# Kernel optimization log

Hardware: AMD Instinct MI355X
Metric: run time of the kernel (lower is better)

## Reference

```python
import jax, jax.numpy as jnp
import numpy as np

# Static problem constants (see shape_source)
T_, H_, W_ = 8, 37, 37          # frames, feature-map height/width (518/14)
NH, MP = 8, 8                   # num_heads, max_points


def _point_mask_np():
    # n_points(t, r) = max(1, int(MP * (1 - |t-r|/(T-1)))) as in the TxT loop.
    d = np.abs(np.arange(T_)[:, None] - np.arange(T_)[None, :])
    n_p = np.maximum(1, (MP * (1.0 - d / (T_ - 1))).astype(np.int64))
    return np.arange(MP)[None, None, :] < n_p[:, :, None]   # [T, T, P] bool


def setup_inputs() -> dict:
    key = jax.random.key(0)
    ks = jax.random.split(key, 4)
    B, T, N, C = 2, T_, H_ * W_, 384
    f_bt = jax.random.normal(ks[0], (B, T, N, C), jnp.float32)
    Wq = 0.05 * jax.random.normal(ks[1], (C, C), jnp.float32)
    Woff = 0.1 * jax.random.normal(ks[2], (C, NH * MP * 2), jnp.float32)  # offsets span a few pixels
    Wout = 0.05 * jax.random.normal(ks[3], (C, C), jnp.float32)
    return {
        'f_bt': f_bt,
        'Wq': Wq, 'bq': jnp.zeros((C,), jnp.float32),
        'Woff': Woff, 'boff': jnp.zeros((NH * MP * 2,), jnp.float32),
        'Wout': Wout, 'bout': jnp.zeros((C,), jnp.float32),
    }


def _forward(f_bt, Wq, bq, Woff, boff, Wout, bout):
    B, T, N, C = f_bt.shape
    h, P = NH, MP
    hd = C // h
    scale = hd ** -0.5
    H, W = H_, W_

    # Per-frame projections (query and offsets depend only on t, computed once).
    q = (f_bt @ Wq + bq).reshape(B, T, N, h, hd)                 # [B,T,N,h,hd]
    off = (f_bt @ Woff + boff).reshape(B, T, N, h, P, 2)         # [B,T,N,h,P,2]

    ys, xs = jnp.meshgrid(jnp.arange(H), jnp.arange(W), indexing='ij')
    coords = jnp.stack([ys, xs], -1).reshape(N, 2).astype(f_bt.dtype)
    # Sampling locations in pixel space (align_corners=True normalize+denormalize is identity).
    loc = coords[None, None, :, None, None, :] + off             # [B,T,N,h,P,2]

    # Reference frames as per-head channel images, flattened spatially.
    ref = f_bt.transpose(0, 1, 3, 2).reshape(B, T, h, hd, N)     # [B,T,h,hd,H*W]
    mask = jnp.asarray(_point_mask_np())                         # [T,T,P]

    def attend(q_t, loc_t, mask_t):
        # q_t: [B,N,h,hd], loc_t: [B,N,h,P,2], mask_t: [T,P]
        y = loc_t[..., 0]
        x = loc_t[..., 1]
        y0f = jnp.floor(y)
        x0f = jnp.floor(x)
        wy = y - y0f
        wx = x - x0f

        def gather(yf, xf, w):
            yi = yf.astype(jnp.int32)
            xi = xf.astype(jnp.int32)
            valid = ((yi >= 0) & (yi < H) & (xi >= 0) & (xi < W)).astype(q_t.dtype)
            idx = jnp.clip(yi, 0, H - 1) * W + jnp.clip(xi, 0, W - 1)     # [B,N,h,P]
            idx = idx.transpose(0, 2, 1, 3).reshape(B, 1, h, 1, N * P)
            idx = jnp.broadcast_to(idx, (B, T, h, 1, N * P))
            vals = jnp.take_along_axis(ref, idx, axis=4)                   # [B,T,h,hd,N*P]
            vals = vals.reshape(B, T, h, hd, N, P)
            wv = (w * valid).transpose(0, 2, 1, 3)[:, None, :, None, :, :]  # [B,1,h,1,N,P]
            return vals * wv

        # Bilinear sample (zeros padding) of every reference frame at the
        # offset-predicted points of frame t.
        s = (gather(y0f, x0f, (1 - wy) * (1 - wx))
             + gather(y0f, x0f + 1, (1 - wy) * wx)
             + gather(y0f + 1, x0f, wy * (1 - wx))
             + gather(y0f + 1, x0f + 1, wy * wx))                # [B,T,h,hd,N,P]

        logits = jnp.einsum('bnhd,brhdnp->brnhp', q_t, s) * scale
        logits = logits + jnp.where(mask_t[None, :, None, None, :], 0.0, -1e30)
        attn = jax.nn.softmax(logits, axis=-1)
        out = jnp.einsum('brnhp,brhdnp->brnhd', attn, s).mean(axis=1)  # avg over T refs
        return out.reshape(B, N, C) @ Wout + bout

    body = jax.checkpoint(attend)

    def step(carry, xs):
        q_t, loc_t, mask_t = xs
        return carry, body(q_t, loc_t, mask_t)

    _, fused = jax.lax.scan(
        step, None,
        (q.transpose(1, 0, 2, 3, 4), loc.transpose(1, 0, 2, 3, 4, 5), mask))
    return fused.transpose(1, 0, 2, 3)   # [B,T,N,C]


def reference(f_bt, Wq, bq, Woff, boff, Wout, bout):
    return _forward(f_bt, Wq, bq, Woff, boff, Wout, bout)
```

## Files before the change

kernel.cpp:

```cpp
#include <hip/hip_runtime.h>
#include <hip/hip_bf16.h>
#include <hip/hip_fp16.h>
#include <cstddef>

constexpr int B_  = 2;
constexpr int T_  = 8;
constexpr int HW_ = 37;
constexpr int N_  = HW_ * HW_;
constexpr int C_  = 384;
constexpr int NH_ = 8;
constexpr int MP_ = 8;
constexpr int HD_ = C_ / NH_;
constexpr int M_  = B_ * T_ * N_;

typedef short bf16x8 __attribute__((ext_vector_type(8)));
typedef float f32x4 __attribute__((ext_vector_type(4)));
typedef float f32x2 __attribute__((ext_vector_type(2)));
typedef _Float16 h16x2 __attribute__((ext_vector_type(2)));
typedef unsigned u32x3 __attribute__((ext_vector_type(3)));
typedef u32x3 uau32x3 __attribute__((aligned(4)));

static __device__ __forceinline__ unsigned short bf16_bits(float v) {
  __hip_bfloat16 b = __float2bfloat16(v);
  return *reinterpret_cast<unsigned short*>(&b);
}

static __device__ __forceinline__ h16x2 bch2(unsigned u) {
  return __builtin_bit_cast(h16x2, u);
}

__global__ __launch_bounds__(256)
void cast_transpose_kernel(const float* __restrict__ f,
                           __hip_bfloat16* __restrict__ A16,
                           _Float16* __restrict__ fth) {
  const int bn = blockIdx.x;
  const int n = bn % N_;
  const int b = bn / N_;
#pragma unroll
  for (int i = 0; i < 12; ++i) {
    int idx = i * 256 + threadIdx.x;
    int t = idx / C_;
    int c = idx - t * C_;
    int h = c / HD_;
    int c48 = c - h * HD_;
    size_t src = ((size_t)(b * T_ + t) * N_ + n) * C_ + c;
    float v = f[src];
    fth[(((size_t)(b * NH_ + h) * N_ + n) * T_ + t) * HD_ + c48] = (_Float16)v;
    A16[src] = __float2bfloat16(v);
  }
}

__global__ __launch_bounds__(256)
void prep_w_kernel(const float* __restrict__ Wq, const float* __restrict__ Woff,
                   const float* __restrict__ Wout,
                   __hip_bfloat16* __restrict__ Wt, __hip_bfloat16* __restrict__ Wot) {
  int nrow = blockIdx.x;
  if (nrow < 512) {
    const float* src; int col, ld;
    if (nrow < 384) { src = Wq; col = nrow; ld = 384; }
    else            { src = Woff; col = nrow - 384; ld = 128; }
    for (int k = threadIdx.x; k < 384; k += 256)
      Wt[(size_t)nrow * 384 + k] = __float2bfloat16(src[(size_t)k * ld + col]);
  } else {
    int col = nrow - 512;
    for (int k = threadIdx.x; k < 384; k += 256)
      Wot[(size_t)col * 384 + k] = __float2bfloat16(Wout[(size_t)k * 384 + col]);
  }
}

__global__ __launch_bounds__(256)
void mfma_gemm_kernel(const __hip_bfloat16* __restrict__ A,
                      const __hip_bfloat16* __restrict__ Wt,
                      const float* __restrict__ b0, const float* __restrict__ b1,
                      float* __restrict__ out0, _Float16* __restrict__ out0h,
                      float* __restrict__ out1,
                      int split, float out0_scale) {
  __shared__ __hip_bfloat16 As[128][40];
  __shared__ __hip_bfloat16 Bs[128][40];
  const int m0 = blockIdx.x * 128;
  const int n0 = blockIdx.y * 128;
  const int tid = threadIdx.x;
  const int wv = tid >> 6, lane = tid & 63;
  const int wr = wv >> 1, wc = wv & 1;
  const int lr = lane & 15, kg = lane >> 4;

  f32x4 acc[4][4] = {};

  for (int k0 = 0; k0 < 384; k0 += 32) {
#pragma unroll
    for (int u = 0; u < 2; ++u) {
      int c = tid + u * 256;
      int row = c >> 2;
      int off = (c & 3) * 8;
      int gm = m0 + row;
      uint4 va = make_uint4(0u, 0u, 0u, 0u);
      if (gm < M_) va = *(const uint4*)(A + (size_t)gm * 384 + k0 + off);
      *(uint4*)&As[row][off] = va;
      uint4 vb = *(const uint4*)(Wt + (size_t)(n0 + row) * 384 + k0 + off);
      *(uint4*)&Bs[row][off] = vb;
    }
    __syncthreads();

    bf16x8 af[4], bfr[4];
#pragma unroll
    for (int i = 0; i < 4; ++i)
      af[i] = *(const bf16x8*)&As[wr * 64 + i * 16 + lr][kg * 8];
#pragma unroll
    for (int i = 0; i < 4; ++i)
      bfr[i] = *(const bf16x8*)&Bs[wc * 64 + i * 16 + lr][kg * 8];

#pragma unroll
    for (int mi = 0; mi < 4; ++mi)
#pragma unroll
      for (int ni = 0; ni < 4; ++ni)
        acc[mi][ni] = __builtin_amdgcn_mfma_f32_16x16x32_bf16(
            af[mi], bfr[ni], acc[mi][ni], 0, 0, 0);
    __syncthreads();
  }

  const int mrow = (lane >> 4) * 4;
#pragma unroll
  for (int mi = 0; mi < 4; ++mi) {
#pragma unroll
    for (int ni = 0; ni < 4; ++ni) {
#pragma unroll
      for (int j = 0; j < 4; ++j) {
        int gm = m0 + wr * 64 + mi * 16 + mrow + j;
        int gn = n0 + wc * 64 + ni * 16 + lr;
        if (gm >= M_) continue;
        float v = acc[mi][ni][j];
        if (!split) {
          out0[(size_t)gm * 384 + gn] = (v + b0[gn]) * out0_scale;
        } else {
          if (gn < 384) out0h[(size_t)gm * 384 + gn] =
              (_Float16)((v + b0[gn]) * out0_scale);
          else          out1[(size_t)gm * 128 + (gn - 384)] = v + b1[gn - 384];
        }
      }
    }
  }
}

__global__ __launch_bounds__(256)
void attend_kernel(const _Float16* __restrict__ fth,
                   const _Float16* __restrict__ Qh,
                   const float* __restrict__ OFF,
                   __hip_bfloat16* __restrict__ O1) {
  const int grid = B_ * N_ * 2;
  const int q8 = grid / 8, r8 = grid % 8;
  int c = blockIdx.x & 7, j = blockIdx.x >> 3;
  int id = (c < r8) ? c * (q8 + 1) + j : r8 * (q8 + 1) + (c - r8) * q8 + j;
  const int hq = id & 1;
  const int bn = id >> 1;

  const int n = bn % N_;
  const int b = bn / N_;
  const int w    = threadIdx.x >> 6;
  const int h    = hq * 4 + w;
  const int lane = threadIdx.x & 63;
  const int r = lane >> 3;
  const int k = lane & 7;
  const float cy = (float)(n / HW_);
  const float cx = (float)(n % HW_);

  const _Float16* fh = fth + (size_t)(b * NH_ + h) * N_ * (T_ * HD_);
  const int laneoff = lane * 6;

  for (int t = 0; t < T_; ++t) {
    const size_t row = (size_t)(b * T_ + t) * N_ + n;

    uau32x3 qw = *(const uau32x3*)(Qh + row * C_ + h * HD_ + 6 * k);
    h16x2 q01 = bch2(qw.x), q23 = bch2(qw.y), q45 = bch2(qw.z);

    int dd = t - r; dd = dd < 0 ? -dd : dd;
    const int npts = max(1, (56 - 8 * dd) / 7);

    const float* opb = OFF + row * (NH_ * MP_ * 2) + h * (MP_ * 2);

    float o0 = 0.f, o1 = 0.f, o2 = 0.f, o3 = 0.f, o4 = 0.f, o5 = 0.f;
    float esum = 0.f;

#pragma unroll
    for (int p = 0; p < MP_; ++p) {
      float y = cy + opb[2 * p];
      float x = cx + opb[2 * p + 1];
      float y0f = floorf(y), x0f = floorf(x);
      float wy = y - y0f, wx = x - x0f;
      int y0 = (int)y0f, x0 = (int)x0f;
      int y1 = y0 + 1, x1 = x0 + 1;
      float vy0 = (y0 >= 0 && y0 < HW_) ? 1.f : 0.f;
      float vy1 = (y1 >= 0 && y1 < HW_) ? 1.f : 0.f;
      float vx0 = (x0 >= 0 && x0 < HW_) ? 1.f : 0.f;
      float vx1 = (x1 >= 0 && x1 < HW_) ? 1.f : 0.f;
      int cy0 = min(max(y0, 0), HW_ - 1), cy1 = min(max(y1, 0), HW_ - 1);
      int cx0 = min(max(x0, 0), HW_ - 1), cx1 = min(max(x1, 0), HW_ - 1);
      float tw0 = (1.f - wy) * (1.f - wx) * vy0 * vx0;
      float tw1 = (1.f - wy) * wx * vy0 * vx1;
      float tw2 = wy * (1.f - wx) * vy1 * vx0;
      float tw3 = wy * wx * vy1 * vx1;
      _Float16 t0h = (_Float16)tw0, t1h = (_Float16)tw1;
      _Float16 t2h = (_Float16)tw2, t3h = (_Float16)tw3;
      h16x2 tw0h = {t0h, t0h}, tw1h = {t1h, t1h};
      h16x2 tw2h = {t2h, t2h}, tw3h = {t3h, t3h};

      const _Float16* g0 = fh + (size_t)(cy0 * HW_ + cx0) * (T_ * HD_) + laneoff;
      const _Float16* g1 = fh + (size_t)(cy0 * HW_ + cx1) * (T_ * HD_) + laneoff;
      const _Float16* g2 = fh + (size_t)(cy1 * HW_ + cx0) * (T_ * HD_) + laneoff;
      const _Float16* g3 = fh + (size_t)(cy1 * HW_ + cx1) * (T_ * HD_) + laneoff;
      uau32x3 ua = *(const uau32x3*)g0;
      uau32x3 ub = *(const uau32x3*)g1;
      uau32x3 uc = *(const uau32x3*)g2;
      uau32x3 ud = *(const uau32x3*)g3;

      h16x2 s01 = bch2(ua.x) * tw0h + bch2(ub.x) * tw1h + bch2(uc.x) * tw2h + bch2(ud.x) * tw3h;
      h16x2 s23 = bch2(ua.y) * tw0h + bch2(ub.y) * tw1h + bch2(uc.y) * tw2h + bch2(ud.y) * tw3h;
      h16x2 s45 = bch2(ua.z) * tw0h + bch2(ub.z) * tw1h + bch2(uc.z) * tw2h + bch2(ud.z) * tw3h;

      float lg = __builtin_amdgcn_fdot2(q01, s01,
                 __builtin_amdgcn_fdot2(q23, s23,
                 __builtin_amdgcn_fdot2(q45, s45, 0.f, false), false), false);
      lg += __shfl_xor(lg, 1);
      lg += __shfl_xor(lg, 2);
      lg += __shfl_xor(lg, 4);

      float e = (p < npts) ? exp2f(lg) : 0.f;
      esum += e;

      o0 = fmaf((float)s01.x, e, o0);
      o1 = fmaf((float)s01.y, e, o1);
      o2 = fmaf((float)s23.x, e, o2);
      o3 = fmaf((float)s23.y, e, o3);
      o4 = fmaf((float)s45.x, e, o4);
      o5 = fmaf((float)s45.y, e, o5);
    }

    float inv = __builtin_amdgcn_rcpf(esum);
    o0 *= inv; o1 *= inv; o2 *= inv; o3 *= inv; o4 *= inv; o5 *= inv;

    o0 += __shfl_xor(o0, 8); o0 += __shfl_xor(o0, 16); o0 += __shfl_xor(o0, 32);
    o1 += __shfl_xor(o1, 8); o1 += __shfl_xor(o1, 16); o1 += __shfl_xor(o1, 32);
    o2 += __shfl_xor(o2, 8); o2 += __shfl_xor(o2, 16); o2 += __shfl_xor(o2, 32);
    o3 += __shfl_xor(o3, 8); o3 += __shfl_xor(o3, 16); o3 += __shfl_xor(o3, 32);
    o4 += __shfl_xor(o4, 8); o4 += __shfl_xor(o4, 16); o4 += __shfl_xor(o4, 32);
    o5 += __shfl_xor(o5, 8); o5 += __shfl_xor(o5, 16); o5 += __shfl_xor(o5, 32);

    if (r == 0) {
      __hip_bfloat16* outp = O1 + row * C_ + h * HD_ + 6 * k;
      unsigned* u = (unsigned*)outp;
      u[0] = (unsigned)bf16_bits(o0 * 0.125f) | ((unsigned)bf16_bits(o1 * 0.125f) << 16);
      u[1] = (unsigned)bf16_bits(o2 * 0.125f) | ((unsigned)bf16_bits(o3 * 0.125f) << 16);
      u[2] = (unsigned)bf16_bits(o4 * 0.125f) | ((unsigned)bf16_bits(o5 * 0.125f) << 16);
    }
  }
}

extern "C" void kernel_launch(void* const* d_in, const int* in_sizes, int n_in,
                              void* d_out, int out_size, void* d_ws, size_t ws_size,
                              hipStream_t stream) {
  const float* f    = (const float*)d_in[0];
  const float* Wq   = (const float*)d_in[1];
  const float* bq   = (const float*)d_in[2];
  const float* Woff = (const float*)d_in[3];
  const float* boff = (const float*)d_in[4];
  const float* Wout = (const float*)d_in[5];
  const float* bout = (const float*)d_in[6];
  float* outp = (float*)d_out;

  _Float16* Qh = (_Float16*)d_ws;
  float* OFFb = (float*)(Qh + (size_t)M_ * C_);
  _Float16* fth = (_Float16*)(OFFb + (size_t)M_ * 128);
  __hip_bfloat16* A16 = (__hip_bfloat16*)(fth + (size_t)B_ * N_ * T_ * C_);
  __hip_bfloat16* O1  = A16;
  __hip_bfloat16* Wt  = A16 + (size_t)M_ * C_;
  __hip_bfloat16* Wot = Wt + (size_t)512 * 384;

  dim3 blk(256);

  cast_transpose_kernel<<<dim3(B_ * N_), blk, 0, stream>>>(f, A16, fth);
  prep_w_kernel<<<dim3(896), blk, 0, stream>>>(Wq, Woff, Wout, Wt, Wot);

  mfma_gemm_kernel<<<dim3((M_ + 127) / 128, 4), blk, 0, stream>>>(
      A16, Wt, bq, boff, nullptr, Qh, OFFb, 1, 0.20822825268806912f);

  attend_kernel<<<dim3(B_ * N_ * 2), blk, 0, stream>>>(fth, Qh, OFFb, O1);

  mfma_gemm_kernel<<<dim3((M_ + 127) / 128, 3), blk, 0, stream>>>(
      O1, Wot, bout, nullptr, outp, nullptr, nullptr, 0, 1.0f);
}
```

Measured before the change: 312.4 us.

## Precompute bilinear tap indices and weights in a separate kernel, store offsets as fp16

Adds a prep kernel that turns each sampling offset into four packed 16-bit pixel indices and four fp16 bilinear weights, computed once per (row, head, point). The attend kernel previously redid this per reference frame in every lane; it now loads one uint4 per point instead. The offset GEMM output becomes fp16, halving its footprint. In exchange there is an extra launch, a roughly 22 MB intermediate buffer to write and read, and reduced precision for the offsets.

```diff
diff --git a/kernel.cpp b/kernel.cpp
--- a/kernel.cpp
+++ b/kernel.cpp
@@ -15,7 +15,6 @@
 
 typedef short bf16x8 __attribute__((ext_vector_type(8)));
 typedef float f32x4 __attribute__((ext_vector_type(4)));
-typedef float f32x2 __attribute__((ext_vector_type(2)));
 typedef _Float16 h16x2 __attribute__((ext_vector_type(2)));
 typedef unsigned u32x3 __attribute__((ext_vector_type(3)));
 typedef u32x3 uau32x3 __attribute__((aligned(4)));
@@ -27,6 +26,10 @@
 
 static __device__ __forceinline__ h16x2 bch2(unsigned u) {
   return __builtin_bit_cast(h16x2, u);
+}
+
+static __device__ __forceinline__ unsigned h2u(h16x2 v) {
+  return __builtin_bit_cast(unsigned, v);
 }
 
 __global__ __launch_bounds__(256)
@@ -73,7 +76,7 @@
                       const __hip_bfloat16* __restrict__ Wt,
                       const float* __restrict__ b0, const float* __restrict__ b1,
                       float* __restrict__ out0, _Float16* __restrict__ out0h,
-                      float* __restrict__ out1,
+                      _Float16* __restrict__ out1,
                       int split, float out0_scale) {
   __shared__ __hip_bfloat16 As[128][40];
   __shared__ __hip_bfloat16 Bs[128][40];
@@ -134,7 +137,8 @@
         } else {
           if (gn < 384) out0h[(size_t)gm * 384 + gn] =
               (_Float16)((v + b0[gn]) * out0_scale);
-          else          out1[(size_t)gm * 128 + (gn - 384)] = v + b1[gn - 384];
+          else          out1[(size_t)gm * 128 + (gn - 384)] =
+              (_Float16)(v + b1[gn - 384]);
         }
       }
     }
@@ -142,9 +146,44 @@
 }
 
 __global__ __launch_bounds__(256)
+void prep_tap_kernel(const _Float16* __restrict__ OFFh, uint4* __restrict__ prec) {
+  int gid = blockIdx.x * 256 + threadIdx.x;
+  int row = gid >> 6;
+  int hp = gid & 63;
+  int n = row % N_;
+  float cy = (float)(n / HW_);
+  float cx = (float)(n % HW_);
+  h16x2 off = *(const h16x2*)(OFFh + (size_t)row * 128 + hp * 2);
+  float y = cy + (float)off.x;
+  float x = cx + (float)off.y;
+  float y0f = floorf(y), x0f = floorf(x);
+  float wy = y - y0f, wx = x - x0f;
+  int y0 = (int)y0f, x0 = (int)x0f;
+  int y1 = y0 + 1, x1 = x0 + 1;
+  float vy0 = (y0 >= 0 && y0 < HW_) ? 1.f : 0.f;
+  float vy1 = (y1 >= 0 && y1 < HW_) ? 1.f : 0.f;
+  float vx0 = (x0 >= 0 && x0 < HW_) ? 1.f : 0.f;
+  float vx1 = (x1 >= 0 && x1 < HW_) ? 1.f : 0.f;
+  int cy0 = min(max(y0, 0), HW_ - 1), cy1 = min(max(y1, 0), HW_ - 1);
+  int cx0 = min(max(x0, 0), HW_ - 1), cx1 = min(max(x1, 0), HW_ - 1);
+  float w00 = (1.f - wy) * (1.f - wx) * vy0 * vx0;
+  float w01 = (1.f - wy) * wx * vy0 * vx1;
+  float w10 = wy * (1.f - wx) * vy1 * vx0;
+  float w11 = wy * wx * vy1 * vx1;
+  uint4 o;
+  o.x = (unsigned)(cy0 * HW_ + cx0) | ((unsigned)(cy0 * HW_ + cx1) << 16);
+  o.y = (unsigned)(cy1 * HW_ + cx0) | ((unsigned)(cy1 * HW_ + cx1) << 16);
+  h16x2 wa = {(_Float16)w00, (_Float16)w01};
+  h16x2 wb = {(_Float16)w10, (_Float16)w11};
+  o.z = h2u(wa);
+  o.w = h2u(wb);
+  prec[gid] = o;
+}
+
+__global__ __launch_bounds__(256)
 void attend_kernel(const _Float16* __restrict__ fth,
                    const _Float16* __restrict__ Qh,
-                   const float* __restrict__ OFF,
+                   const uint4* __restrict__ prec,
                    __hip_bfloat16* __restrict__ O1) {
   const int grid = B_ * N_ * 2;
   const int q8 = grid / 8, r8 = grid % 8;
@@ -160,8 +199,6 @@
   const int lane = threadIdx.x & 63;
   const int r = lane >> 3;
   const int k = lane & 7;
-  const float cy = (float)(n / HW_);
-  const float cx = (float)(n % HW_);
 
   const _Float16* fh = fth + (size_t)(b * NH_ + h) * N_ * (T_ * HD_);
   const int laneoff = lane * 6;
@@ -175,42 +212,24 @@
     int dd = t - r; dd = dd < 0 ? -dd : dd;
     const int npts = max(1, (56 - 8 * dd) / 7);
 
-    const float* opb = OFF + row * (NH_ * MP_ * 2) + h * (MP_ * 2);
+    const uint4* precrow = prec + ((size_t)row * 8 + h) * 8;
 
     float o0 = 0.f, o1 = 0.f, o2 = 0.f, o3 = 0.f, o4 = 0.f, o5 = 0.f;
     float esum = 0.f;
 
 #pragma unroll
     for (int p = 0; p < MP_; ++p) {
-      float y = cy + opb[2 * p];
-      float x = cx + opb[2 * p + 1];
-      float y0f = floorf(y), x0f = floorf(x);
-      float wy = y - y0f, wx = x - x0f;
-      int y0 = (int)y0f, x0 = (int)x0f;
-      int y1 = y0 + 1, x1 = x0 + 1;
-      float vy0 = (y0 >= 0 && y0 < HW_) ? 1.f : 0.f;
-      float vy1 = (y1 >= 0 && y1 < HW_) ? 1.f : 0.f;
-      float vx0 = (x0 >= 0 && x0 < HW_) ? 1.f : 0.f;
-      float vx1 = (x1 >= 0 && x1 < HW_) ? 1.f : 0.f;
-      int cy0 = min(max(y0, 0), HW_ - 1), cy1 = min(max(y1, 0), HW_ - 1);
-      int cx0 = min(max(x0, 0), HW_ - 1), cx1 = min(max(x1, 0), HW_ - 1);
-      float tw0 = (1.f - wy) * (1.f - wx) * vy0 * vx0;
-      float tw1 = (1.f - wy) * wx * vy0 * vx1;
-      float tw2 = wy * (1.f - wx) * vy1 * vx0;
-      float tw3 = wy * wx * vy1 * vx1;
-      _Float16 t0h = (_Float16)tw0, t1h = (_Float16)tw1;
-      _Float16 t2h = (_Float16)tw2, t3h = (_Float16)tw3;
-      h16x2 tw0h = {t0h, t0h}, tw1h = {t1h, t1h};
-      h16x2 tw2h = {t2h, t2h}, tw3h = {t3h, t3h};
-
-      const _Float16* g0 = fh + (size_t)(cy0 * HW_ + cx0) * (T_ * HD_) + laneoff;
-      const _Float16* g1 = fh + (size_t)(cy0 * HW_ + cx1) * (T_ * HD_) + laneoff;
-      const _Float16* g2 = fh + (size_t)(cy1 * HW_ + cx0) * (T_ * HD_) + laneoff;
-      const _Float16* g3 = fh + (size_t)(cy1 * HW_ + cx1) * (T_ * HD_) + laneoff;
-      uau32x3 ua = *(const uau32x3*)g0;
-      uau32x3 ub = *(const uau32x3*)g1;
-      uau32x3 uc = *(const uau32x3*)g2;
-      uau32x3 ud = *(const uau32x3*)g3;
+      uint4 pr = precrow[p];
+      int i00 = pr.x & 0xffff, i01 = pr.x >> 16;
+      int i10 = pr.y & 0xffff, i11 = pr.y >> 16;
+      h16x2 wa = bch2(pr.z), wb = bch2(pr.w);
+      h16x2 tw0h = {wa.x, wa.x}, tw1h = {wa.y, wa.y};
+      h16x2 tw2h = {wb.x, wb.x}, tw3h = {wb.y, wb.y};
+
+      uau32x3 ua = *(const uau32x3*)(fh + i00 * (T_ * HD_) + laneoff);
+      uau32x3 ub = *(const uau32x3*)(fh + i01 * (T_ * HD_) + laneoff);
+      uau32x3 uc = *(const uau32x3*)(fh + i10 * (T_ * HD_) + laneoff);
+      uau32x3 ud = *(const uau32x3*)(fh + i11 * (T_ * HD_) + laneoff);
 
       h16x2 s01 = bch2(ua.x) * tw0h + bch2(ub.x) * tw1h + bch2(uc.x) * tw2h + bch2(ud.x) * tw3h;
       h16x2 s23 = bch2(ua.y) * tw0h + bch2(ub.y) * tw1h + bch2(uc.y) * tw2h + bch2(ud.y) * tw3h;
@@ -267,12 +286,13 @@
   float* outp = (float*)d_out;
 
   _Float16* Qh = (_Float16*)d_ws;
-  float* OFFb = (float*)(Qh + (size_t)M_ * C_);
-  _Float16* fth = (_Float16*)(OFFb + (size_t)M_ * 128);
+  _Float16* OFFh = Qh + (size_t)M_ * C_;
+  _Float16* fth = OFFh + (size_t)M_ * 128;
   __hip_bfloat16* A16 = (__hip_bfloat16*)(fth + (size_t)B_ * N_ * T_ * C_);
   __hip_bfloat16* O1  = A16;
   __hip_bfloat16* Wt  = A16 + (size_t)M_ * C_;
   __hip_bfloat16* Wot = Wt + (size_t)512 * 384;
+  uint4* prec = (uint4*)(Wot + (size_t)384 * 384);
 
   dim3 blk(256);
 
@@ -280,9 +300,11 @@
   prep_w_kernel<<<dim3(896), blk, 0, stream>>>(Wq, Woff, Wout, Wt, Wot);
 
   mfma_gemm_kernel<<<dim3((M_ + 127) / 128, 4), blk, 0, stream>>>(
-      A16, Wt, bq, boff, nullptr, Qh, OFFb, 1, 0.20822825268806912f);
-
-  attend_kernel<<<dim3(B_ * N_ * 2), blk, 0, stream>>>(fth, Qh, OFFb, O1);
+      A16, Wt, bq, boff, nullptr, Qh, OFFh, 1, 0.20822825268806912f);
+
+  prep_tap_kernel<<<dim3(M_ / 4), blk, 0, stream>>>(OFFh, prec);
+
+  attend_kernel<<<dim3(B_ * N_ * 2), blk, 0, stream>>>(fth, Qh, prec, O1);
 
   mfma_gemm_kernel<<<dim3((M_ + 127) / 128, 3), blk, 0, stream>>>(
       O1, Wot, bout, nullptr, outp, nullptr, nullptr, 0, 1.0f);
```

New measurement: 290.5 us. -7.0%, faster.
